# Kernel tuning notes

Hardware: AMD Instinct MI355X
Metric: run time of the kernel (lower is better)

Reference implementation:

```python
import jax, jax.numpy as jnp
import numpy as np

NUM_ITERATIONS = 3


def squash(v, axis=-1):
    sq = jnp.sum(v * v, axis=axis, keepdims=True)
    scale = sq / (1.0 + sq)
    return scale * v / jnp.sqrt(sq)


def setup_inputs() -> dict:
    key = jax.random.key(0)
    k1, k2 = jax.random.split(key)
    B, N, IN, OUT, CAPS = 512, 4608, 16, 32, 32
    x = jax.random.normal(k1, (B, N, IN), dtype=jnp.float32)
    # torch.rand -> uniform [0, 1)
    route_weights = jax.random.uniform(k2, (N, IN, OUT), dtype=jnp.float32)
    return {"x": x, "route_weights": route_weights, "num_capsules": CAPS}


def reference(x, route_weights, num_capsules):
    # x: [B, N, IN], route_weights: [N, IN, OUT]
    u_hat = jnp.einsum('bnk,nkl->bnl', x, route_weights)  # [B, N, OUT]
    N = x.shape[1]
    b = jnp.zeros((N, num_capsules), dtype=u_hat.dtype)  # routing logits [N, CAPS]
    v = None
    for it in range(NUM_ITERATIONS):
        c = jax.nn.softmax(b, axis=-1)                     # [N, CAPS]
        s = jnp.einsum('bnk,nc->bck', u_hat, c)            # [B, CAPS, OUT]
        v = squash(s, axis=-1)                             # [B, CAPS, OUT]
        if it < NUM_ITERATIONS - 1:
            b = b + jnp.einsum('bnk,bck->nc', u_hat, v)    # agreement, reduced over batch
    return v
```

## Files before the change

kernel.cpp:

```cpp
#include <hip/hip_runtime.h>


#define NB 512
#define KTOT 73728
#define OUTC 32
#define NCAPS 32

#define KSPLIT 128
#define KCHUNK (KTOT / KSPLIT)
#define NSTEP (KCHUNK / 32)
#define SPA_BYTES ((size_t)KSPLIT * NB * OUTC * 4)
#define S_BYTES ((size_t)NB * OUTC * 4)

typedef short bf16x8 __attribute__((ext_vector_type(8)));
typedef float f32x4 __attribute__((ext_vector_type(4)));

__device__ __forceinline__ unsigned int f2bf(float f) {
    union { float f; unsigned int u; } v; v.f = f;
    unsigned int u = v.u;
    return (u + 0x7fffu + ((u >> 16) & 1u)) >> 16;
}

template <bool PART>
__global__ __launch_bounds__(256) void gemm_mfma(
        const float* __restrict__ x, const float* __restrict__ w,
        float* __restrict__ S) {
    __shared__ __align__(16) unsigned short wl[NSTEP * 1024];
    const int t = threadIdx.x;
    const int lane = t & 63;
    const int wave = t >> 6;
    const int bx = blockIdx.x;
    const int by = blockIdx.y;
    const size_t kbase = (size_t)bx * KCHUNK;

    for (int tt = t; tt < NSTEP * 128; tt += 256) {
        int ll = tt & 63;
        int h = (tt >> 6) & 1;
        int step = tt >> 7;
        int k0 = step * 32 + ((ll >> 4) & 3) * 8;
        int c = h * 16 + (ll & 15);
        const float* wp0 = w + (kbase + (size_t)k0) * OUTC + c;
        unsigned int u[4];
#pragma unroll
        for (int j = 0; j < 4; ++j) {
            unsigned int lo = f2bf(wp0[(2 * j) * OUTC]);
            unsigned int hi = f2bf(wp0[(2 * j + 1) * OUTC]);
            u[j] = lo | (hi << 16);
        }
        *(uint4*)&wl[(size_t)tt * 8] = make_uint4(u[0], u[1], u[2], u[3]);
    }
    __syncthreads();

    const int row0 = by * 64 + wave * 16;
    const int m = lane & 15;
    const int q = lane >> 4;

    const float* xp = x + (size_t)(row0 + m) * KTOT + kbase + q * 8;
    const unsigned short* wp = wl + lane * 8;

    f32x4 acc0 = {0.f, 0.f, 0.f, 0.f};
    f32x4 acc1 = {0.f, 0.f, 0.f, 0.f};

#pragma unroll 6
    for (int s = 0; s < NSTEP; ++s) {
        float4 xa = *(const float4*)xp;
        float4 xb = *(const float4*)(xp + 4);
        xp += 32;
        bf16x8 b0 = *(const bf16x8*)(wp);
        bf16x8 b1 = *(const bf16x8*)(wp + 512);
        wp += 1024;
        bf16x8 a;
        a[0] = (short)f2bf(xa.x); a[1] = (short)f2bf(xa.y);
        a[2] = (short)f2bf(xa.z); a[3] = (short)f2bf(xa.w);
        a[4] = (short)f2bf(xb.x); a[5] = (short)f2bf(xb.y);
        a[6] = (short)f2bf(xb.z); a[7] = (short)f2bf(xb.w);
        acc0 = __builtin_amdgcn_mfma_f32_16x16x32_bf16(a, b0, acc0, 0, 0, 0);
        acc1 = __builtin_amdgcn_mfma_f32_16x16x32_bf16(a, b1, acc1, 0, 0, 0);
    }

#pragma unroll
    for (int r = 0; r < 4; ++r) {
        const int row = row0 + q * 4 + r;
        if (PART) {
            float* dst = S + ((size_t)bx * NB + row) * OUTC;
            dst[m] = acc0[r];
            dst[16 + m] = acc1[r];
        } else {
            atomicAdd(&S[(size_t)row * OUTC + m], acc0[r]);
            atomicAdd(&S[(size_t)row * OUTC + 16 + m], acc1[r]);
        }
    }
}

__global__ __launch_bounds__(256) void zero_s(float* __restrict__ S) {
    int i = blockIdx.x * 256 + threadIdx.x;
    if (i < NB * OUTC) S[i] = 0.0f;
}

__global__ __launch_bounds__(256) void finalize2(const float* __restrict__ S,
                                                 float* __restrict__ out) {
    __shared__ float sm[8][32];
    const int b = blockIdx.x;
    const int t = threadIdx.x;
    const int k = t & 31;
    const int g = t >> 5;
    const float* sp = S + ((size_t)(g * 16) * NB + b) * OUTC + k;
    float a = 0.0f;
#pragma unroll 16
    for (int i = 0; i < 16; ++i)
        a += sp[(size_t)i * NB * OUTC];
    sm[g][k] = a;
    __syncthreads();
    float tot = 0.0f;
#pragma unroll
    for (int gg = 0; gg < 8; ++gg) tot += sm[gg][k];
    float s = tot * (1.0f / 32.0f);
    float sq = s * s;
    sq += __shfl_xor(sq, 16, 64);
    sq += __shfl_xor(sq, 8, 64);
    sq += __shfl_xor(sq, 4, 64);
    sq += __shfl_xor(sq, 2, 64);
    sq += __shfl_xor(sq, 1, 64);
    float scale = sq / ((1.0f + sq) * sqrtf(sq));
    float v = s * scale;
    float* orow = out + (size_t)b * (NCAPS * OUTC);
#pragma unroll
    for (int j = 0; j < 4; ++j)
        orow[(g * 4 + j) * OUTC + k] = v;
}

__global__ __launch_bounds__(64) void finalize_k(const float* __restrict__ S,
                                                 float* __restrict__ out) {
    const int b = blockIdx.x;
    const int t = threadIdx.x;
    const int k = t & 31;
    const int h = t >> 5;
    float s = S[(size_t)b * OUTC + k] * (1.0f / 32.0f);
    float sq = s * s;
    sq += __shfl_xor(sq, 16, 64);
    sq += __shfl_xor(sq, 8, 64);
    sq += __shfl_xor(sq, 4, 64);
    sq += __shfl_xor(sq, 2, 64);
    sq += __shfl_xor(sq, 1, 64);
    float scale = sq / ((1.0f + sq) * sqrtf(sq));
    float v = s * scale;
    float* orow = out + (size_t)b * (NCAPS * OUTC);
#pragma unroll
    for (int j = 0; j < 16; ++j)
        orow[(h + j * 2) * OUTC + k] = v;
}

#define FKSPLIT 64
#define FKCHUNK 1152
#define FKT 128
#define FNQ 32
#define FRPW 2
#define FKSTR 132

__global__ __launch_bounds__(256) void gemm_fb(
        const float* __restrict__ x, const float* __restrict__ w,
        float* __restrict__ S) {
    __shared__ float wlds[OUTC * FKSTR];
    const int t = threadIdx.x;
    const int lane = t & 63;
    const int l32 = lane & 31;
    const int half = lane >> 5;
    const int wave = t >> 6;
    const int row0 = blockIdx.x * 16 + wave * 4 + half * FRPW;
    const size_t kbase = (size_t)blockIdx.y * FKCHUNK;
    const int sc = t & 31;
    const int sh = t >> 5;

    float acc[FRPW][OUTC];
#pragma unroll
    for (int r = 0; r < FRPW; ++r)
#pragma unroll
        for (int c = 0; c < OUTC; ++c) acc[r][c] = 0.0f;

    const float4* xq[FRPW];
#pragma unroll
    for (int r = 0; r < FRPW; ++r)
        xq[r] = (const float4*)(x + (size_t)(row0 + r) * KTOT + kbase);

    for (int tile = 0; tile < FKCHUNK / FKT; ++tile) {
        float4 xv[FRPW];
#pragma unroll
        for (int r = 0; r < FRPW; ++r)
            xv[r] = xq[r][tile * FNQ + l32];
#pragma unroll
        for (int jj = 0; jj < 4; ++jj) {
            int kk = 4 * (jj * 8 + sh);
            const float* wg = w + (kbase + (size_t)tile * FKT + kk) * OUTC + sc;
            *(float4*)&wlds[sc * FKSTR + kk] =
                make_float4(wg[0], wg[OUTC], wg[2 * OUTC], wg[3 * OUTC]);
        }
        __syncthreads();
#pragma unroll
        for (int c = 0; c < OUTC; ++c) {
            float4 wv = *(const float4*)&wlds[c * FKSTR + 4 * l32];
#pragma unroll
            for (int r = 0; r < FRPW; ++r) {
                float a = acc[r][c];
                a = fmaf(xv[r].x, wv.x, a);
                a = fmaf(xv[r].y, wv.y, a);
                a = fmaf(xv[r].z, wv.z, a);
                a = fmaf(xv[r].w, wv.w, a);
                acc[r][c] = a;
            }
        }
        __syncthreads();
    }
#pragma unroll
    for (int r = 0; r < FRPW; ++r) {
        float myv = 0.0f;
#pragma unroll
        for (int c = 0; c < OUTC; ++c) {
            float v = acc[r][c];
            v += __shfl_xor(v, 16, 64);
            v += __shfl_xor(v, 8, 64);
            v += __shfl_xor(v, 4, 64);
            v += __shfl_xor(v, 2, 64);
            v += __shfl_xor(v, 1, 64);
            if (l32 == c) myv = v;
        }
        atomicAdd(&S[(size_t)(row0 + r) * OUTC + l32], myv);
    }
}

extern "C" void kernel_launch(void* const* d_in, const int* in_sizes, int n_in,
                              void* d_out, int out_size, void* d_ws, size_t ws_size,
                              hipStream_t stream) {
    const float* x = (const float*)d_in[0];
    const float* w = (const float*)d_in[1];
    float* out = (float*)d_out;

    if (ws_size >= SPA_BYTES) {
        float* S = (float*)d_ws;
        hipLaunchKernelGGL((gemm_mfma<true>), dim3(KSPLIT, 8), dim3(256), 0,
                           stream, x, w, S);
        hipLaunchKernelGGL(finalize2, dim3(NB), dim3(256), 0, stream, S, out);
    } else if (ws_size >= S_BYTES) {
        float* S = (float*)d_ws;
        hipLaunchKernelGGL(zero_s, dim3((NB * OUTC + 255) / 256), dim3(256), 0,
                           stream, S);
        hipLaunchKernelGGL((gemm_mfma<false>), dim3(KSPLIT, 8), dim3(256), 0,
                           stream, x, w, S);
        hipLaunchKernelGGL(finalize_k, dim3(NB), dim3(64), 0, stream, S, out);
    } else {
        float* S = (float*)d_ws;
        hipLaunchKernelGGL(zero_s, dim3((NB * OUTC + 255) / 256), dim3(256), 0,
                           stream, S);
        hipLaunchKernelGGL(gemm_fb, dim3(32, FKSPLIT), dim3(256), 0, stream,
                           x, w, S);
        hipLaunchKernelGGL(finalize_k, dim3(NB), dim3(64), 0, stream, S, out);
    }
}
```

Baseline: 230.8 us.

## Stage x and w tiles through LDS with register-prefetch software pipelining

Replaces the up-front staging of the whole w chunk in LDS, and the direct per-lane x loads, with a tiled loop over 64-wide K tiles. Each tile of both x and w is loaded cooperatively into registers, converted to bf16, and stored to LDS, while the next tile's global loads are issued before the barrier. The aim is coalesced x loads and overlap of global memory latency with MFMA work, and it also cuts LDS per block. The cost is two barriers per tile, extra LDS traffic for x, and only two MFMA steps per tile to hide that sync overhead.

```diff
diff --git a/kernel.cpp b/kernel.cpp
--- a/kernel.cpp
+++ b/kernel.cpp
@@ -8,7 +8,7 @@
 
 #define KSPLIT 128
 #define KCHUNK (KTOT / KSPLIT)
-#define NSTEP (KCHUNK / 32)
+#define NTILE 9
 #define SPA_BYTES ((size_t)KSPLIT * NB * OUTC * 4)
 #define S_BYTES ((size_t)NB * OUTC * 4)
 
@@ -25,59 +25,84 @@
 __global__ __launch_bounds__(256) void gemm_mfma(
         const float* __restrict__ x, const float* __restrict__ w,
         float* __restrict__ S) {
-    __shared__ __align__(16) unsigned short wl[NSTEP * 1024];
+    __shared__ __align__(16) unsigned short wl[2048];
+    __shared__ __align__(16) unsigned short xl[4096];
     const int t = threadIdx.x;
     const int lane = t & 63;
     const int wave = t >> 6;
     const int bx = blockIdx.x;
     const int by = blockIdx.y;
+    const int brow = by * 64;
     const size_t kbase = (size_t)bx * KCHUNK;
 
-    for (int tt = t; tt < NSTEP * 128; tt += 256) {
-        int ll = tt & 63;
-        int h = (tt >> 6) & 1;
-        int step = tt >> 7;
-        int k0 = step * 32 + ((ll >> 4) & 3) * 8;
-        int c = h * 16 + (ll & 15);
-        const float* wp0 = w + (kbase + (size_t)k0) * OUTC + c;
-        unsigned int u[4];
-#pragma unroll
-        for (int j = 0; j < 4; ++j) {
-            unsigned int lo = f2bf(wp0[(2 * j) * OUTC]);
-            unsigned int hi = f2bf(wp0[(2 * j + 1) * OUTC]);
-            u[j] = lo | (hi << 16);
-        }
-        *(uint4*)&wl[(size_t)tt * 8] = make_uint4(u[0], u[1], u[2], u[3]);
-    }
-    __syncthreads();
-
-    const int row0 = by * 64 + wave * 16;
     const int m = lane & 15;
     const int q = lane >> 4;
 
-    const float* xp = x + (size_t)(row0 + m) * KTOT + kbase + q * 8;
-    const unsigned short* wp = wl + lane * 8;
+    const int sm_ = t & 15;
+    const int sr_ = t >> 4;
+    const int xsl = sm_ >> 3;
+    const int xq  = (sm_ >> 1) & 3;
+    const int xj0 = (sm_ & 1) * 4;
+    const int ll  = t & 63;
+    const int h   = (t >> 6) & 1;
+    const int slw = t >> 7;
+    const int wk0 = slw * 32 + ((ll >> 4) & 3) * 8;
+    const int wc  = h * 16 + (ll & 15);
 
     f32x4 acc0 = {0.f, 0.f, 0.f, 0.f};
     f32x4 acc1 = {0.f, 0.f, 0.f, 0.f};
 
-#pragma unroll 6
-    for (int s = 0; s < NSTEP; ++s) {
-        float4 xa = *(const float4*)xp;
-        float4 xb = *(const float4*)(xp + 4);
-        xp += 32;
-        bf16x8 b0 = *(const bf16x8*)(wp);
-        bf16x8 b1 = *(const bf16x8*)(wp + 512);
-        wp += 1024;
-        bf16x8 a;
-        a[0] = (short)f2bf(xa.x); a[1] = (short)f2bf(xa.y);
-        a[2] = (short)f2bf(xa.z); a[3] = (short)f2bf(xa.w);
-        a[4] = (short)f2bf(xb.x); a[5] = (short)f2bf(xb.y);
-        a[6] = (short)f2bf(xb.z); a[7] = (short)f2bf(xb.w);
-        acc0 = __builtin_amdgcn_mfma_f32_16x16x32_bf16(a, b0, acc0, 0, 0, 0);
-        acc1 = __builtin_amdgcn_mfma_f32_16x16x32_bf16(a, b1, acc1, 0, 0, 0);
-    }
-
+    float  wr[8];
+    float4 xr[4];
+
+    {
+        const float* wp0 = w + (kbase + (size_t)wk0) * OUTC + wc;
+#pragma unroll
+        for (int j = 0; j < 8; ++j) wr[j] = wp0[(size_t)j * OUTC];
+        const float* xb = x + kbase + sm_ * 4;
+#pragma unroll
+        for (int ld = 0; ld < 4; ++ld)
+            xr[ld] = *(const float4*)(xb + (size_t)(brow + sr_ + ld * 16) * KTOT);
+    }
+
+    for (int tile = 0; tile < NTILE; ++tile) {
+        {
+            unsigned int u0 = f2bf(wr[0]) | (f2bf(wr[1]) << 16);
+            unsigned int u1 = f2bf(wr[2]) | (f2bf(wr[3]) << 16);
+            unsigned int u2 = f2bf(wr[4]) | (f2bf(wr[5]) << 16);
+            unsigned int u3 = f2bf(wr[6]) | (f2bf(wr[7]) << 16);
+            *(uint4*)&wl[t * 8] = make_uint4(u0, u1, u2, u3);
+#pragma unroll
+            for (int ld = 0; ld < 4; ++ld) {
+                unsigned int a0 = f2bf(xr[ld].x) | (f2bf(xr[ld].y) << 16);
+                unsigned int a1 = f2bf(xr[ld].z) | (f2bf(xr[ld].w) << 16);
+                *(uint2*)&xl[((ld * 2 + xsl) * 16 + sr_) * 32 + xq * 8 + xj0] =
+                    make_uint2(a0, a1);
+            }
+        }
+        if (tile + 1 < NTILE) {
+            const size_t kt = kbase + (size_t)(tile + 1) * 64;
+            const float* wp0 = w + (kt + (size_t)wk0) * OUTC + wc;
+#pragma unroll
+            for (int j = 0; j < 8; ++j) wr[j] = wp0[(size_t)j * OUTC];
+            const float* xb = x + kt + sm_ * 4;
+#pragma unroll
+            for (int ld = 0; ld < 4; ++ld)
+                xr[ld] = *(const float4*)(xb + (size_t)(brow + sr_ + ld * 16) * KTOT);
+        }
+        __syncthreads();
+#pragma unroll
+        for (int sl = 0; sl < 2; ++sl) {
+            bf16x8 a  = *(const bf16x8*)&xl[((wave * 2 + sl) * 16 + m) * 32 + q * 8];
+            bf16x8 b0 = *(const bf16x8*)&wl[sl * 1024 + lane * 8];
+            bf16x8 b1 = *(const bf16x8*)&wl[sl * 1024 + 512 + lane * 8];
+            acc0 = __builtin_amdgcn_mfma_f32_16x16x32_bf16(a, b0, acc0, 0, 0, 0);
+            acc1 = __builtin_amdgcn_mfma_f32_16x16x32_bf16(a, b1, acc1, 0, 0, 0);
+        }
+        __syncthreads();
+    }
+
+    const int row0 = brow + wave * 16;
 #pragma unroll
     for (int r = 0; r < 4; ++r) {
         const int row = row0 + q * 4 + r;
```

After: 224.3 us. 2.8% less time.
